# Performance work log

Hardware: AMD Instinct MI355X
Metric: run time of the kernel (lower is better)

## Reference

```python
import jax, jax.numpy as jnp
import numpy as np

C = 256        # in_channels
HEADS = 8
HD = 64        # dim_heads
INNER = HEADS * HD   # 512
G = 32         # norm_groups
FF = 4 * INNER # 2048
EPS = 1e-5


def setup_inputs() -> dict:
    key = jax.random.key(0)
    ks = jax.random.split(key, 12)
    r = lambda k, shp: jax.random.normal(k, shp, jnp.float32) * 0.02
    return {
        "x": jax.random.normal(ks[0], (1, C, 16, 16, 16), jnp.float32),
        "gn_g": jnp.ones((C,), jnp.float32),
        "gn_b": jnp.zeros((C,), jnp.float32),
        "w_in": r(ks[1], (INNER, C)),   # Conv3d 1x1x1 as (out,in) matrix
        "b_in": jnp.zeros((INNER,), jnp.float32),
        "wq": r(ks[2], (INNER, INNER)),
        "wk": r(ks[3], (INNER, INNER)),
        "wv": r(ks[4], (INNER, INNER)),
        "ln1_g": jnp.ones((INNER,), jnp.float32),
        "ln1_b": jnp.zeros((INNER,), jnp.float32),
        "ff_w1": r(ks[5], (FF, INNER)),
        "ff_b1": jnp.zeros((FF,), jnp.float32),
        "ff_w2": r(ks[6], (INNER, FF)),
        "ff_b2": jnp.zeros((INNER,), jnp.float32),
        "ln2_g": jnp.ones((INNER,), jnp.float32),
        "ln2_b": jnp.zeros((INNER,), jnp.float32),
        "w_out": r(ks[7], (C, INNER)),  # Conv3d 1x1x1 back to C
        "b_out": jnp.zeros((C,), jnp.float32),
    }


def _group_norm(x, g, b):
    # x: (B,C,D,H,W), G groups, normalize over (C//G, D, H, W)
    B, Cc, D, H, W = x.shape
    xr = x.reshape(B, G, Cc // G, D, H, W)
    mu = jnp.mean(xr, axis=(2, 3, 4, 5), keepdims=True)
    var = jnp.var(xr, axis=(2, 3, 4, 5), keepdims=True)
    xr = (xr - mu) * jax.lax.rsqrt(var + EPS)
    xn = xr.reshape(B, Cc, D, H, W)
    return xn * g[None, :, None, None, None] + b[None, :, None, None, None]


def _layer_norm(x, g, b):
    mu = jnp.mean(x, axis=-1, keepdims=True)
    var = jnp.var(x, axis=-1, keepdims=True)
    return (x - mu) * jax.lax.rsqrt(var + EPS) * g + b


def reference(x, gn_g, gn_b, w_in, b_in, wq, wk, wv, ln1_g, ln1_b,
              ff_w1, ff_b1, ff_w2, ff_b2, ln2_g, ln2_b, w_out, b_out):
    B, Cc, D, H, W = x.shape
    x_in = x
    # GroupNorm + proj_in (1x1x1 conv == channel matmul)
    h = _group_norm(x, gn_g, gn_b)
    t = jnp.einsum('bcdhw,oc->bodhw', h, w_in) + b_in[None, :, None, None, None]
    N = D * H * W
    t = t.reshape(B, INNER, N).transpose(0, 2, 1)  # (B, N, INNER)

    # self-attention (manual einsum softmax einsum)
    q = (t @ wq.T).reshape(B, N, HEADS, HD)
    k = (t @ wk.T).reshape(B, N, HEADS, HD)
    v = (t @ wv.T).reshape(B, N, HEADS, HD)
    scale = HD ** (-0.5)
    scores = jnp.einsum('bihd,bjhd->bhij', q, k) * scale  # (B,H,N,N)
    attn = jax.nn.softmax(scores, axis=-1)
    o = jnp.einsum('bhij,bjhd->bihd', attn, v).reshape(B, N, INNER)
    # out_proj is Identity (q_dim == inner_dim), dropout=0
    t = _layer_norm(o + t, ln1_g, ln1_b)

    # FeedForward: Linear -> GELU (erf) -> Linear
    ff = jax.nn.gelu(t @ ff_w1.T + ff_b1, approximate=False) @ ff_w2.T + ff_b2
    t = _layer_norm(ff + t, ln2_g, ln2_b)

    # proj_out + residual
    y = t.transpose(0, 2, 1).reshape(B, INNER, D, H, W)
    out = jnp.einsum('bidhw,oi->bodhw', y, w_out) + b_out[None, :, None, None, None]
    return out + x_in
```

## Files before the change

kernel.cpp:

```cpp
#include <hip/hip_runtime.h>
#include <hip/hip_bf16.h>

typedef unsigned short u16;
typedef __attribute__((ext_vector_type(8))) short short8;
typedef __attribute__((ext_vector_type(4))) float floatx4;

#define LOG2E 1.44269504088896f
#define CEXP (0.125f * LOG2E)

static __device__ __forceinline__ u16 f2b(float f) {
  union { float f; unsigned u; } v; v.f = f;
  unsigned r = v.u + 0x7fffu + ((v.u >> 16) & 1u);
  return (u16)(r >> 16);
}
static __device__ __forceinline__ float b2f(u16 b) {
  union { float f; unsigned u; } v; v.u = ((unsigned)b) << 16;
  return v.f;
}
static __device__ __forceinline__ void async16(const u16* g, u16* l) {
  __builtin_amdgcn_global_load_lds(
      (const __attribute__((address_space(1))) unsigned int*)g,
      (__attribute__((address_space(3))) unsigned int*)l, 16, 0, 0);
}
static __device__ __forceinline__ float fexp2(float x) {
  return __builtin_amdgcn_exp2f(x);
}

__global__ __launch_bounds__(256) void f2b_all(
    const float* __restrict__ s0, const float* __restrict__ s1, const float* __restrict__ s2,
    const float* __restrict__ s3, const float* __restrict__ s4, const float* __restrict__ s5,
    const float* __restrict__ s6, const float* __restrict__ x,
    u16* __restrict__ d_win, u16* __restrict__ d_qkv, u16* __restrict__ d_f1,
    u16* __restrict__ d_f2, u16* __restrict__ d_wout, float2* __restrict__ cstats) {
  if (blockIdx.x >= 12288) {
    int c = blockIdx.x - 12288;
    const float4* p4 = (const float4*)(x + (size_t)c * 4096);
    float s = 0.f, ss = 0.f;
#pragma unroll
    for (int j = 0; j < 4; j++) {
      float4 v = p4[j * 256 + threadIdx.x];
      s += v.x + v.y + v.z + v.w;
      ss += v.x * v.x + v.y * v.y + v.z * v.z + v.w * v.w;
    }
    for (int m = 1; m < 64; m <<= 1) { s += __shfl_xor(s, m); ss += __shfl_xor(ss, m); }
    __shared__ float sb[8];
    int w = threadIdx.x >> 6;
    if ((threadIdx.x & 63) == 0) { sb[w * 2] = s; sb[w * 2 + 1] = ss; }
    __syncthreads();
    if (threadIdx.x == 0)
      cstats[c] = float2{sb[0] + sb[2] + sb[4] + sb[6], sb[1] + sb[3] + sb[5] + sb[7]};
    return;
  }
  int i = blockIdx.x * 256 + threadIdx.x;
  if (i < 131072) { d_win[i] = f2b(s0[i]); return; }
  i -= 131072;
  if (i < 262144) { d_qkv[i] = f2b(s1[i]); return; }
  i -= 262144;
  if (i < 262144) { d_qkv[262144 + i] = f2b(s2[i]); return; }
  i -= 262144;
  if (i < 262144) { d_qkv[524288 + i] = f2b(s3[i]); return; }
  i -= 262144;
  if (i < 1048576) { d_f1[i] = f2b(s4[i]); return; }
  i -= 1048576;
  if (i < 1048576) { d_f2[i] = f2b(s5[i]); return; }
  i -= 1048576;
  d_wout[i] = f2b(s6[i]);
}

__global__ __launch_bounds__(256) void gn_apply(const float* __restrict__ x, const float2* __restrict__ cstats,
                                                const float* __restrict__ gg, const float* __restrict__ gb,
                                                u16* __restrict__ hn) {
  __shared__ float tile[256 * 17];
  __shared__ float gmu[32], grs[32];
  int t = threadIdx.x;
  if (t < 32) {
    float s = 0.f, ss = 0.f;
#pragma unroll
    for (int j = 0; j < 8; j++) { float2 p = cstats[t * 8 + j]; s += p.x; ss += p.y; }
    float mu = s / 32768.f;
    gmu[t] = mu;
    grs[t] = rsqrtf(ss / 32768.f - mu * mu + 1e-5f);
  }
  __syncthreads();
  int n0 = blockIdx.x * 16;
#pragma unroll
  for (int j = 0; j < 4; j++) {
    int c = j * 64 + (t >> 2);
    int nl = (t & 3) * 4;
    float4 v = *(const float4*)&x[(size_t)c * 4096 + n0 + nl];
    float ga = gg[c] * grs[c >> 3];
    float bb = gb[c] - gmu[c >> 3] * ga;
    tile[c * 17 + nl + 0] = v.x * ga + bb;
    tile[c * 17 + nl + 1] = v.y * ga + bb;
    tile[c * 17 + nl + 2] = v.z * ga + bb;
    tile[c * 17 + nl + 3] = v.w * ga + bb;
  }
  __syncthreads();
#pragma unroll
  for (int j = 0; j < 16; j++)
    hn[(size_t)(n0 + j) * 256 + t] = f2b(tile[t * 17 + j]);
}

#define FLAG_BIAS 1
#define FLAG_GELU 2
#define FLAG_C16 8
#define FLAG_FINAL 32
#define FLAG_CZ 64

__global__ __launch_bounds__(256) void gemm_bt(
    const u16* __restrict__ A, const u16* __restrict__ B, const float* __restrict__ bias,
    float* __restrict__ C32, u16* __restrict__ C16, const float* __restrict__ resid,
    int M, int N, int K, int flags) {
  __shared__ u16 As[128 * 64];
  __shared__ u16 Bs[64 * 64];
  const int t = threadIdx.x;
  const int lane = t & 63;
  const int w = t >> 6;
  const int ln = lane & 15;
  const int quad = lane >> 4;
  const int m0 = blockIdx.x * 128;
  const int n0 = blockIdx.y * 64;
  const int wm = (w >> 1) * 64;
  const int wn = (w & 1) * 32;

  floatx4 acc[4][2];
#pragma unroll
  for (int i = 0; i < 4; i++)
#pragma unroll
    for (int j = 0; j < 2; j++) acc[i][j] = floatx4{0.f, 0.f, 0.f, 0.f};

  for (int k0 = 0; k0 < K; k0 += 64) {
    __syncthreads();
#pragma unroll
    for (int i = 0; i < 4; ++i) {
      int s = i * 256 + t;
      int row = s >> 3;
      int kb = (s & 7) ^ (row & 7);
      async16(A + (size_t)(m0 + row) * K + k0 + kb * 8, &As[(i * 256 + (t & ~63)) * 8]);
    }
#pragma unroll
    for (int i = 0; i < 2; ++i) {
      int s = i * 256 + t;
      int row = s >> 3;
      int kb = (s & 7) ^ (row & 7);
      async16(B + (size_t)(n0 + row) * K + k0 + kb * 8, &Bs[(i * 256 + (t & ~63)) * 8]);
    }
    __syncthreads();
#pragma unroll
    for (int ksi = 0; ksi < 2; ksi++) {
      short8 af[4], bfr[2];
      int kb = ksi * 4 + quad;
#pragma unroll
      for (int i = 0; i < 4; i++) {
        int m = wm + i * 16 + ln;
        af[i] = *(const short8*)&As[(m * 8 + (kb ^ (m & 7))) * 8];
      }
#pragma unroll
      for (int j = 0; j < 2; j++) {
        int n = wn + j * 16 + ln;
        bfr[j] = *(const short8*)&Bs[(n * 8 + (kb ^ (n & 7))) * 8];
      }
#pragma unroll
      for (int i = 0; i < 4; i++)
#pragma unroll
        for (int j = 0; j < 2; j++)
          acc[i][j] = __builtin_amdgcn_mfma_f32_16x16x32_bf16(af[i], bfr[j], acc[i][j], 0, 0, 0);
    }
  }

#pragma unroll
  for (int i = 0; i < 4; i++) {
#pragma unroll
    for (int j = 0; j < 2; j++) {
      int n = n0 + wn + j * 16 + ln;
      float bv = (flags & FLAG_BIAS) ? bias[n] : 0.f;
#pragma unroll
      for (int r = 0; r < 4; r++) {
        int m = m0 + wm + i * 16 + quad * 4 + r;
        float v = acc[i][j][r] + bv;
        if (flags & FLAG_C16) C16[(size_t)m * N + n] = f2b(v);
        if (flags & FLAG_FINAL)
          C32[(size_t)m * N + n] = v + bias[m] + resid[(size_t)m * N + n];
      }
    }
  }
}

__global__ __launch_bounds__(256) void gemm_big(
    const u16* __restrict__ A, const u16* __restrict__ B, const float* __restrict__ bias,
    u16* __restrict__ C16, int M, int N, int K, int flags) {
  __shared__ u16 As[128 * 64];
  __shared__ u16 Bs[128 * 64];
  const int t = threadIdx.x;
  const int lane = t & 63;
  const int w = t >> 6;
  const int ln = lane & 15;
  const int quad = lane >> 4;
  const int m0 = blockIdx.x * 128;
  const int n0 = blockIdx.y * 128;
  const int wm = (w >> 1) * 64;
  const int wn = (w & 1) * 64;
  const int kper = K / gridDim.z;
  const int kbeg = blockIdx.z * kper;

  floatx4 acc[4][4];
#pragma unroll
  for (int i = 0; i < 4; i++)
#pragma unroll
    for (int j = 0; j < 4; j++) acc[i][j] = floatx4{0.f, 0.f, 0.f, 0.f};

  for (int k0 = kbeg; k0 < kbeg + kper; k0 += 64) {
    __syncthreads();
#pragma unroll
    for (int i = 0; i < 4; ++i) {
      int s = i * 256 + t;
      int row = s >> 3;
      int kb = (s & 7) ^ (row & 7);
      async16(A + (size_t)(m0 + row) * K + k0 + kb * 8, &As[(i * 256 + (t & ~63)) * 8]);
      async16(B + (size_t)(n0 + row) * K + k0 + kb * 8, &Bs[(i * 256 + (t & ~63)) * 8]);
    }
    __syncthreads();
#pragma unroll
    for (int ksi = 0; ksi < 2; ksi++) {
      short8 af[4], bfr[4];
      int kb = ksi * 4 + quad;
#pragma unroll
      for (int i = 0; i < 4; i++) {
        int m = wm + i * 16 + ln;
        af[i] = *(const short8*)&As[(m * 8 + (kb ^ (m & 7))) * 8];
        int n = wn + i * 16 + ln;
        bfr[i] = *(const short8*)&Bs[(n * 8 + (kb ^ (n & 7))) * 8];
      }
#pragma unroll
      for (int i = 0; i < 4; i++)
#pragma unroll
        for (int j = 0; j < 4; j++)
          acc[i][j] = __builtin_amdgcn_mfma_f32_16x16x32_bf16(af[i], bfr[j], acc[i][j], 0, 0, 0);
    }
  }

  u16* Cdst = (flags & FLAG_CZ) ? C16 + (size_t)blockIdx.z * M * N : C16;
#pragma unroll
  for (int i = 0; i < 4; i++) {
#pragma unroll
    for (int j = 0; j < 4; j++) {
      int n = n0 + wn + j * 16 + ln;
      float bv = ((flags & FLAG_BIAS) && blockIdx.z == 0) ? bias[n] : 0.f;
#pragma unroll
      for (int r = 0; r < 4; r++) {
        int m = m0 + wm + i * 16 + quad * 4 + r;
        float v = acc[i][j][r] + bv;
        if (flags & FLAG_GELU) v = 0.5f * v * (1.f + erff(v * 0.70710678118f));
        Cdst[(size_t)m * N + n] = f2b(v);
      }
    }
  }
}

__global__ __launch_bounds__(256) void gemm_qk(
    const u16* __restrict__ A, const u16* __restrict__ B,
    u16* __restrict__ Cq, u16* __restrict__ Ck, int M, int K) {
  __shared__ u16 As[64 * 64];
  __shared__ u16 Bs[128 * 64];
  const int t = threadIdx.x;
  const int lane = t & 63;
  const int w = t >> 6;
  const int ln = lane & 15;
  const int quad = lane >> 4;
  const int m0 = blockIdx.x * 64;
  const int n0 = blockIdx.y * 128;
  const int wm = (w >> 1) * 32;
  const int wn = (w & 1) * 64;

  floatx4 acc[2][4];
#pragma unroll
  for (int i = 0; i < 2; i++)
#pragma unroll
    for (int j = 0; j < 4; j++) acc[i][j] = floatx4{0.f, 0.f, 0.f, 0.f};

  for (int k0 = 0; k0 < K; k0 += 64) {
    __syncthreads();
#pragma unroll
    for (int i = 0; i < 2; ++i) {
      int s = i * 256 + t;
      int row = s >> 3;
      int kb = (s & 7) ^ (row & 7);
      async16(A + (size_t)(m0 + row) * K + k0 + kb * 8, &As[(i * 256 + (t & ~63)) * 8]);
    }
#pragma unroll
    for (int i = 0; i < 4; ++i) {
      int s = i * 256 + t;
      int row = s >> 3;
      int kb = (s & 7) ^ (row & 7);
      async16(B + (size_t)(n0 + row) * K + k0 + kb * 8, &Bs[(i * 256 + (t & ~63)) * 8]);
    }
    __syncthreads();
#pragma unroll
    for (int ksi = 0; ksi < 2; ksi++) {
      short8 af[2], bfr[4];
      int kb = ksi * 4 + quad;
#pragma unroll
      for (int i = 0; i < 2; i++) {
        int m = wm + i * 16 + ln;
        af[i] = *(const short8*)&As[(m * 8 + (kb ^ (m & 7))) * 8];
      }
#pragma unroll
      for (int j = 0; j < 4; j++) {
        int n = wn + j * 16 + ln;
        bfr[j] = *(const short8*)&Bs[(n * 8 + (kb ^ (n & 7))) * 8];
      }
#pragma unroll
      for (int i = 0; i < 2; i++)
#pragma unroll
        for (int j = 0; j < 4; j++)
          acc[i][j] = __builtin_amdgcn_mfma_f32_16x16x32_bf16(af[i], bfr[j], acc[i][j], 0, 0, 0);
    }
  }

#pragma unroll
  for (int i = 0; i < 2; i++) {
#pragma unroll
    for (int j = 0; j < 4; j++) {
      int n = n0 + wn + j * 16 + ln;
#pragma unroll
      for (int r = 0; r < 4; r++) {
        int m = m0 + wm + i * 16 + quad * 4 + r;
        float v = acc[i][j][r];
        if (n < 512) Cq[(size_t)m * 512 + n] = f2b(v * CEXP);
        else Ck[(size_t)m * 512 + (n - 512)] = f2b(v);
      }
    }
  }
}

__global__ __launch_bounds__(256, 4) void attn_kernel(
    const u16* __restrict__ Q, const u16* __restrict__ Km, const u16* __restrict__ VT,
    u16* __restrict__ Opart, float* __restrict__ ML, int Nseq, int kvLen) {
  __shared__ u16 Ks[64 * 64];
  __shared__ u16 Vs[64 * 64];
  __shared__ u16 Ps[4 * 32 * 64];
  const int t = threadIdx.x;
  const int lane = t & 63;
  const int w = t >> 6;
  const int ln = lane & 15;
  const int quad = lane >> 4;
  const int h = blockIdx.y;
  const int q0 = blockIdx.x * 128;
  const int split = blockIdx.z;
  const int kvbase = split * kvLen;
  u16* Opw = Opart + (size_t)split * Nseq * 512;
  u16* Pw = &Ps[w * 32 * 64];

  short8 qf[2][2];
#pragma unroll
  for (int qt = 0; qt < 2; qt++)
#pragma unroll
    for (int ksi = 0; ksi < 2; ksi++)
      qf[qt][ksi] = *(const short8*)&Q[(size_t)(q0 + w * 32 + qt * 16 + ln) * 512 + h * 64 + ksi * 32 + quad * 8];

  floatx4 accO[2][4];
#pragma unroll
  for (int qt = 0; qt < 2; qt++)
#pragma unroll
    for (int td = 0; td < 4; td++) accO[qt][td] = floatx4{0.f, 0.f, 0.f, 0.f};
  float lsum[2] = {0.f, 0.f};

  for (int kv = 0; kv < kvLen; kv += 64) {
    const int kv0 = kvbase + kv;
    __syncthreads();
#pragma unroll
    for (int i = 0; i < 2; ++i) {
      int s = i * 256 + t;
      int row = s >> 3;
      int kb = (s & 7) ^ (row & 7);
      async16(Km + (size_t)(kv0 + row) * 512 + h * 64 + kb * 8, &Ks[(i * 256 + (t & ~63)) * 8]);
      async16(VT + (size_t)(h * 64 + row) * Nseq + kv0 + kb * 8, &Vs[(i * 256 + (t & ~63)) * 8]);
    }
    __syncthreads();

    floatx4 accS[2][4];
#pragma unroll
    for (int qt = 0; qt < 2; qt++)
#pragma unroll
      for (int tj = 0; tj < 4; tj++) accS[qt][tj] = floatx4{0.f, 0.f, 0.f, 0.f};
#pragma unroll
    for (int ksi = 0; ksi < 2; ksi++) {
      int kb = ksi * 4 + quad;
      short8 kf[4];
#pragma unroll
      for (int tj = 0; tj < 4; tj++) {
        int key = tj * 16 + ln;
        kf[tj] = *(const short8*)&Ks[(key * 8 + (kb ^ (key & 7))) * 8];
      }
#pragma unroll
      for (int qt = 0; qt < 2; qt++)
#pragma unroll
        for (int tj = 0; tj < 4; tj++)
          accS[qt][tj] = __builtin_amdgcn_mfma_f32_16x16x32_bf16(kf[tj], qf[qt][ksi], accS[qt][tj], 0, 0, 0);
    }

#pragma unroll
    for (int qt = 0; qt < 2; qt++) {
      int q8 = (qt * 16 + ln) * 8;
#pragma unroll
      for (int tj = 0; tj < 4; tj++) {
        float p0 = fexp2(accS[qt][tj][0]);
        float p1 = fexp2(accS[qt][tj][1]);
        float p2 = fexp2(accS[qt][tj][2]);
        float p3 = fexp2(accS[qt][tj][3]);
        lsum[qt] += (p0 + p1) + (p2 + p3);
        __hip_bfloat162 a01 = __float22bfloat162_rn(float2{p0, p1});
        __hip_bfloat162 a23 = __float22bfloat162_rn(float2{p2, p3});
        uint2 pk;
        pk.x = *(unsigned*)&a01;
        pk.y = *(unsigned*)&a23;
        int kbx = tj * 2 + (quad >> 1);
        *(uint2*)&Pw[(q8 + (kbx ^ (ln & 7))) * 8 + (quad & 1) * 4] = pk;
      }
    }

#pragma unroll
    for (int ksi = 0; ksi < 2; ksi++) {
      int kb = ksi * 4 + quad;
      short8 pf[2];
#pragma unroll
      for (int qt = 0; qt < 2; qt++)
        pf[qt] = *(const short8*)&Pw[((qt * 16 + ln) * 8 + (kb ^ (ln & 7))) * 8];
#pragma unroll
      for (int td = 0; td < 4; td++) {
        int d = td * 16 + ln;
        short8 vf = *(const short8*)&Vs[(d * 8 + (kb ^ (d & 7))) * 8];
#pragma unroll
        for (int qt = 0; qt < 2; qt++)
          accO[qt][td] = __builtin_amdgcn_mfma_f32_16x16x32_bf16(vf, pf[qt], accO[qt][td], 0, 0, 0);
      }
    }
  }

#pragma unroll
  for (int qt = 0; qt < 2; qt++) {
    lsum[qt] += __shfl_xor(lsum[qt], 16);
    lsum[qt] += __shfl_xor(lsum[qt], 32);
  }
#pragma unroll
  for (int qt = 0; qt < 2; qt++) {
    int q = q0 + w * 32 + qt * 16 + ln;
#pragma unroll
    for (int td = 0; td < 4; td++) {
      __hip_bfloat162 p01 = __float22bfloat162_rn(float2{accO[qt][td][0], accO[qt][td][1]});
      __hip_bfloat162 p23 = __float22bfloat162_rn(float2{accO[qt][td][2], accO[qt][td][3]});
      uint2 pk;
      pk.x = *(unsigned*)&p01;
      pk.y = *(unsigned*)&p23;
      *(uint2*)&Opw[(size_t)q * 512 + h * 64 + td * 16 + quad * 4] = pk;
    }
    if (quad == 0)
      ML[((size_t)split * 8 + h) * Nseq + q] = lsum[qt];
  }
}

__global__ __launch_bounds__(256) void ln_attn(
    const u16* __restrict__ Opart, const float* __restrict__ ML,
    const u16* __restrict__ t16, const float* __restrict__ g, const float* __restrict__ be,
    u16* __restrict__ o16) {
  int row = blockIdx.x;
  int t = threadIdx.x;
  size_t base = (size_t)row * 512;
  int c0 = 2 * t;
  int h = c0 >> 6;
  float lt = 0.f;
#pragma unroll
  for (int s = 0; s < 4; s++) lt += ML[((size_t)s * 8 + h) * 4096 + row];
  float a0 = 0.f, a1 = 0.f;
#pragma unroll
  for (int s = 0; s < 4; s++) {
    unsigned oo = *(const unsigned*)&Opart[(size_t)s * 4096 * 512 + base + c0];
    a0 += b2f((u16)(oo & 0xffff));
    a1 += b2f((u16)(oo >> 16));
  }
  unsigned tt = *(const unsigned*)&t16[base + c0];
  float inv = 1.0f / lt;
  float v0 = a0 * inv + b2f((u16)(tt & 0xffff));
  float v1 = a1 * inv + b2f((u16)(tt >> 16));
  float s = v0 + v1, ss = v0 * v0 + v1 * v1;
  for (int m = 1; m < 64; m <<= 1) { s += __shfl_xor(s, m); ss += __shfl_xor(ss, m); }
  __shared__ float sb[8];
  int w = t >> 6;
  if ((t & 63) == 0) { sb[w * 2] = s; sb[w * 2 + 1] = ss; }
  __syncthreads();
  s = sb[0] + sb[2] + sb[4] + sb[6];
  ss = sb[1] + sb[3] + sb[5] + sb[7];
  float mu = s / 512.f;
  float var = ss / 512.f - mu * mu;
  float rs = rsqrtf(var + 1e-5f);
  float2 gv = *(const float2*)&g[c0];
  float2 bv = *(const float2*)&be[c0];
  u16 r0 = f2b((v0 - mu) * rs * gv.x + bv.x);
  u16 r1 = f2b((v1 - mu) * rs * gv.y + bv.y);
  *(unsigned*)&o16[base + c0] = ((unsigned)r1 << 16) | r0;
}

__global__ __launch_bounds__(256) void ln_ff(
    const u16* __restrict__ zp, const u16* __restrict__ u,
    const float* __restrict__ g, const float* __restrict__ be, u16* __restrict__ o16) {
  int row = blockIdx.x;
  int t = threadIdx.x;
  size_t base = (size_t)row * 512;
  int c0 = 2 * t;
  unsigned uu = *(const unsigned*)&u[base + c0];
  float v0 = b2f((u16)(uu & 0xffff));
  float v1 = b2f((u16)(uu >> 16));
#pragma unroll
  for (int z = 0; z < 4; z++) {
    unsigned zz = *(const unsigned*)&zp[(size_t)z * 4096 * 512 + base + c0];
    v0 += b2f((u16)(zz & 0xffff));
    v1 += b2f((u16)(zz >> 16));
  }
  float s = v0 + v1, ss = v0 * v0 + v1 * v1;
  for (int m = 1; m < 64; m <<= 1) { s += __shfl_xor(s, m); ss += __shfl_xor(ss, m); }
  __shared__ float sb[8];
  int w = t >> 6;
  if ((t & 63) == 0) { sb[w * 2] = s; sb[w * 2 + 1] = ss; }
  __syncthreads();
  s = sb[0] + sb[2] + sb[4] + sb[6];
  ss = sb[1] + sb[3] + sb[5] + sb[7];
  float mu = s / 512.f;
  float var = ss / 512.f - mu * mu;
  float rs = rsqrtf(var + 1e-5f);
  float2 gv = *(const float2*)&g[c0];
  float2 bv = *(const float2*)&be[c0];
  u16 r0 = f2b((v0 - mu) * rs * gv.x + bv.x);
  u16 r1 = f2b((v1 - mu) * rs * gv.y + bv.y);
  *(unsigned*)&o16[base + c0] = ((unsigned)r1 << 16) | r0;
}

extern "C" void kernel_launch(void* const* d_in, const int* in_sizes, int n_in,
                              void* d_out, int out_size, void* d_ws, size_t ws_size,
                              hipStream_t stream) {
  const float* x = (const float*)d_in[0];
  const float* gn_g = (const float*)d_in[1];
  const float* gn_b = (const float*)d_in[2];
  const float* w_in = (const float*)d_in[3];
  const float* b_in = (const float*)d_in[4];
  const float* wq = (const float*)d_in[5];
  const float* wk = (const float*)d_in[6];
  const float* wv = (const float*)d_in[7];
  const float* ln1_g = (const float*)d_in[8];
  const float* ln1_b = (const float*)d_in[9];
  const float* ff_w1 = (const float*)d_in[10];
  const float* ff_b1 = (const float*)d_in[11];
  const float* ff_w2 = (const float*)d_in[12];
  const float* ff_b2 = (const float*)d_in[13];
  const float* ln2_g = (const float*)d_in[14];
  const float* ln2_b = (const float*)d_in[15];
  const float* w_out = (const float*)d_in[16];
  const float* b_out = (const float*)d_in[17];
  float* out = (float*)d_out;
  char* ws = (char*)d_ws;

  u16* w_in16 = (u16*)(ws + 0);
  u16* wqkv16 = (u16*)(ws + 262144);
  u16* fw116 = (u16*)(ws + 1835008);
  u16* fw216 = (u16*)(ws + 3932160);
  u16* wout16 = (u16*)(ws + 6029312);
  u16* u16b = (u16*)(ws + 6291456);
  u16* zp = (u16*)(ws + 10485760);
  u16* t16 = (u16*)(ws + 14680064);
  u16* qb = (u16*)(ws + 18874368);
  u16* kb = (u16*)(ws + 23068672);
  u16* vt = (u16*)(ws + 27262976);
  u16* zb = (u16*)(ws + 27262976);
  u16* opart = (u16*)(ws + 31457280);
  u16* g16 = (u16*)(ws + 31457280);
  float* ml = (float*)(ws + 48234496);
  u16* hn = (u16*)(ws + 49283072);
  float2* cstats = (float2*)(ws + 51380224);

  f2b_all<<<12544, 256, 0, stream>>>(w_in, wq, wk, wv, ff_w1, ff_w2, w_out, x,
                                     w_in16, wqkv16, fw116, fw216, wout16, cstats);
  gn_apply<<<256, 256, 0, stream>>>(x, cstats, gn_g, gn_b, hn);

  gemm_bt<<<dim3(32, 8), 256, 0, stream>>>(hn, w_in16, b_in, nullptr, t16, nullptr,
                                           4096, 512, 256, FLAG_BIAS | FLAG_C16);
  gemm_qk<<<dim3(64, 8), 256, 0, stream>>>(t16, wqkv16, qb, kb, 4096, 512);
  gemm_bt<<<dim3(4, 64), 256, 0, stream>>>(wqkv16 + 2 * 512 * 512, t16, nullptr, nullptr, vt, nullptr,
                                           512, 4096, 512, FLAG_C16);
  attn_kernel<<<dim3(32, 8, 4), 256, 0, stream>>>(qb, kb, vt, opart, ml, 4096, 1024);
  ln_attn<<<4096, 256, 0, stream>>>(opart, ml, t16, ln1_g, ln1_b, u16b);
  gemm_big<<<dim3(32, 16), 256, 0, stream>>>(u16b, fw116, ff_b1, g16,
                                             4096, 2048, 512, FLAG_BIAS | FLAG_GELU | FLAG_C16);
  gemm_big<<<dim3(32, 4, 4), 256, 0, stream>>>(g16, fw216, ff_b2, zp,
                                               4096, 512, 2048, FLAG_BIAS | FLAG_CZ);
  ln_ff<<<4096, 256, 0, stream>>>(zp, u16b, ln2_g, ln2_b, zb);
  gemm_bt<<<dim3(2, 64), 256, 0, stream>>>(wout16, zb, b_out, out, nullptr, x,
                                           256, 4096, 512, FLAG_FINAL);
}
```

Baseline: 245.2 us.

## Merge QK and V-transpose GEMMs into one launch; enlarge attention query tile

Fuses the Q/K projection GEMM and the transposed V projection GEMM into a single kernel launch with 768 blocks, where each block picks its operands from its block index. This removes one launch and lets the two GEMMs share the GPU. The attention kernel now handles 256 queries per block (64 per wave) instead of 128, so each K/V tile loaded into LDS is reused across twice as many queries. In exchange the kernel uses more registers and LDS (launch_bounds min-occupancy dropped) and launches half as many blocks (512), which may lower occupancy.

```diff
diff --git a/kernel.cpp b/kernel.cpp
--- a/kernel.cpp
+++ b/kernel.cpp
@@ -257,9 +257,9 @@
   }
 }
 
-__global__ __launch_bounds__(256) void gemm_qk(
-    const u16* __restrict__ A, const u16* __restrict__ B,
-    u16* __restrict__ Cq, u16* __restrict__ Ck, int M, int K) {
+__global__ __launch_bounds__(256) void gemm_qkvt(
+    const u16* __restrict__ T, const u16* __restrict__ Wqkv,
+    u16* __restrict__ Cq, u16* __restrict__ Ck, u16* __restrict__ CvT) {
   __shared__ u16 As[64 * 64];
   __shared__ u16 Bs[128 * 64];
   const int t = threadIdx.x;
@@ -267,8 +267,23 @@
   const int w = t >> 6;
   const int ln = lane & 15;
   const int quad = lane >> 4;
-  const int m0 = blockIdx.x * 64;
-  const int n0 = blockIdx.y * 128;
+  const int bx = blockIdx.x;
+  const bool isv = bx >= 512;
+  const u16* A;
+  const u16* B;
+  int m0, n0;
+  if (!isv) {
+    m0 = (bx >> 3) * 64;
+    n0 = (bx & 7) * 128;
+    A = T;
+    B = Wqkv;
+  } else {
+    int b2 = bx - 512;
+    m0 = (b2 >> 5) * 64;
+    n0 = (b2 & 31) * 128;
+    A = Wqkv + 2 * 512 * 512;
+    B = T;
+  }
   const int wm = (w >> 1) * 32;
   const int wn = (w & 1) * 64;
 
@@ -278,21 +293,21 @@
 #pragma unroll
     for (int j = 0; j < 4; j++) acc[i][j] = floatx4{0.f, 0.f, 0.f, 0.f};
 
-  for (int k0 = 0; k0 < K; k0 += 64) {
+  for (int k0 = 0; k0 < 512; k0 += 64) {
     __syncthreads();
 #pragma unroll
     for (int i = 0; i < 2; ++i) {
       int s = i * 256 + t;
       int row = s >> 3;
       int kb = (s & 7) ^ (row & 7);
-      async16(A + (size_t)(m0 + row) * K + k0 + kb * 8, &As[(i * 256 + (t & ~63)) * 8]);
+      async16(A + (size_t)(m0 + row) * 512 + k0 + kb * 8, &As[(i * 256 + (t & ~63)) * 8]);
     }
 #pragma unroll
     for (int i = 0; i < 4; ++i) {
       int s = i * 256 + t;
       int row = s >> 3;
       int kb = (s & 7) ^ (row & 7);
-      async16(B + (size_t)(n0 + row) * K + k0 + kb * 8, &Bs[(i * 256 + (t & ~63)) * 8]);
+      async16(B + (size_t)(n0 + row) * 512 + k0 + kb * 8, &Bs[(i * 256 + (t & ~63)) * 8]);
     }
     __syncthreads();
 #pragma unroll
@@ -326,44 +341,45 @@
       for (int r = 0; r < 4; r++) {
         int m = m0 + wm + i * 16 + quad * 4 + r;
         float v = acc[i][j][r];
-        if (n < 512) Cq[(size_t)m * 512 + n] = f2b(v * CEXP);
+        if (isv) CvT[(size_t)m * 4096 + n] = f2b(v);
+        else if (n < 512) Cq[(size_t)m * 512 + n] = f2b(v * CEXP);
         else Ck[(size_t)m * 512 + (n - 512)] = f2b(v);
       }
     }
   }
 }
 
-__global__ __launch_bounds__(256, 4) void attn_kernel(
+__global__ __launch_bounds__(256) void attn_kernel(
     const u16* __restrict__ Q, const u16* __restrict__ Km, const u16* __restrict__ VT,
     u16* __restrict__ Opart, float* __restrict__ ML, int Nseq, int kvLen) {
   __shared__ u16 Ks[64 * 64];
   __shared__ u16 Vs[64 * 64];
-  __shared__ u16 Ps[4 * 32 * 64];
+  __shared__ u16 Ps[4 * 64 * 64];
   const int t = threadIdx.x;
   const int lane = t & 63;
   const int w = t >> 6;
   const int ln = lane & 15;
   const int quad = lane >> 4;
   const int h = blockIdx.y;
-  const int q0 = blockIdx.x * 128;
+  const int q0 = blockIdx.x * 256;
   const int split = blockIdx.z;
   const int kvbase = split * kvLen;
   u16* Opw = Opart + (size_t)split * Nseq * 512;
-  u16* Pw = &Ps[w * 32 * 64];
-
-  short8 qf[2][2];
-#pragma unroll
-  for (int qt = 0; qt < 2; qt++)
+  u16* Pw = &Ps[w * 64 * 64];
+
+  short8 qf[4][2];
+#pragma unroll
+  for (int qt = 0; qt < 4; qt++)
 #pragma unroll
     for (int ksi = 0; ksi < 2; ksi++)
-      qf[qt][ksi] = *(const short8*)&Q[(size_t)(q0 + w * 32 + qt * 16 + ln) * 512 + h * 64 + ksi * 32 + quad * 8];
-
-  floatx4 accO[2][4];
-#pragma unroll
-  for (int qt = 0; qt < 2; qt++)
+      qf[qt][ksi] = *(const short8*)&Q[(size_t)(q0 + w * 64 + qt * 16 + ln) * 512 + h * 64 + ksi * 32 + quad * 8];
+
+  floatx4 accO[4][4];
+#pragma unroll
+  for (int qt = 0; qt < 4; qt++)
 #pragma unroll
     for (int td = 0; td < 4; td++) accO[qt][td] = floatx4{0.f, 0.f, 0.f, 0.f};
-  float lsum[2] = {0.f, 0.f};
+  float lsum[4] = {0.f, 0.f, 0.f, 0.f};
 
   for (int kv = 0; kv < kvLen; kv += 64) {
     const int kv0 = kvbase + kv;
@@ -378,36 +394,34 @@
     }
     __syncthreads();
 
-    floatx4 accS[2][4];
-#pragma unroll
-    for (int qt = 0; qt < 2; qt++)
-#pragma unroll
-      for (int tj = 0; tj < 4; tj++) accS[qt][tj] = floatx4{0.f, 0.f, 0.f, 0.f};
+    short8 kf[2][4];
 #pragma unroll
     for (int ksi = 0; ksi < 2; ksi++) {
       int kb = ksi * 4 + quad;
-      short8 kf[4];
 #pragma unroll
       for (int tj = 0; tj < 4; tj++) {
         int key = tj * 16 + ln;
-        kf[tj] = *(const short8*)&Ks[(key * 8 + (kb ^ (key & 7))) * 8];
-      }
-#pragma unroll
-      for (int qt = 0; qt < 2; qt++)
+        kf[ksi][tj] = *(const short8*)&Ks[(key * 8 + (kb ^ (key & 7))) * 8];
+      }
+    }
+
+#pragma unroll
+    for (int qt = 0; qt < 4; qt++) {
+      floatx4 accS[4];
+#pragma unroll
+      for (int tj = 0; tj < 4; tj++) accS[tj] = floatx4{0.f, 0.f, 0.f, 0.f};
+#pragma unroll
+      for (int ksi = 0; ksi < 2; ksi++)
 #pragma unroll
         for (int tj = 0; tj < 4; tj++)
-          accS[qt][tj] = __builtin_amdgcn_mfma_f32_16x16x32_bf16(kf[tj], qf[qt][ksi], accS[qt][tj], 0, 0, 0);
-    }
-
-#pragma unroll
-    for (int qt = 0; qt < 2; qt++) {
+          accS[tj] = __builtin_amdgcn_mfma_f32_16x16x32_bf16(kf[ksi][tj], qf[qt][ksi], accS[tj], 0, 0, 0);
       int q8 = (qt * 16 + ln) * 8;
 #pragma unroll
       for (int tj = 0; tj < 4; tj++) {
-        float p0 = fexp2(accS[qt][tj][0]);
-        float p1 = fexp2(accS[qt][tj][1]);
-        float p2 = fexp2(accS[qt][tj][2]);
-        float p3 = fexp2(accS[qt][tj][3]);
+        float p0 = fexp2(accS[tj][0]);
+        float p1 = fexp2(accS[tj][1]);
+        float p2 = fexp2(accS[tj][2]);
+        float p3 = fexp2(accS[tj][3]);
         lsum[qt] += (p0 + p1) + (p2 + p3);
         __hip_bfloat162 a01 = __float22bfloat162_rn(float2{p0, p1});
         __hip_bfloat162 a23 = __float22bfloat162_rn(float2{p2, p3});
@@ -422,29 +436,29 @@
 #pragma unroll
     for (int ksi = 0; ksi < 2; ksi++) {
       int kb = ksi * 4 + quad;
-      short8 pf[2];
-#pragma unroll
-      for (int qt = 0; qt < 2; qt++)
+      short8 pf[4];
+#pragma unroll
+      for (int qt = 0; qt < 4; qt++)
         pf[qt] = *(const short8*)&Pw[((qt * 16 + ln) * 8 + (kb ^ (ln & 7))) * 8];
 #pragma unroll
       for (int td = 0; td < 4; td++) {
         int d = td * 16 + ln;
         short8 vf = *(const short8*)&Vs[(d * 8 + (kb ^ (d & 7))) * 8];
 #pragma unroll
-        for (int qt = 0; qt < 2; qt++)
+        for (int qt = 0; qt < 4; qt++)
           accO[qt][td] = __builtin_amdgcn_mfma_f32_16x16x32_bf16(vf, pf[qt], accO[qt][td], 0, 0, 0);
       }
     }
   }
 
 #pragma unroll
-  for (int qt = 0; qt < 2; qt++) {
+  for (int qt = 0; qt < 4; qt++) {
     lsum[qt] += __shfl_xor(lsum[qt], 16);
     lsum[qt] += __shfl_xor(lsum[qt], 32);
   }
 #pragma unroll
-  for (int qt = 0; qt < 2; qt++) {
-    int q = q0 + w * 32 + qt * 16 + ln;
+  for (int qt = 0; qt < 4; qt++) {
+    int q = q0 + w * 64 + qt * 16 + ln;
 #pragma unroll
     for (int td = 0; td < 4; td++) {
       __hip_bfloat162 p01 = __float22bfloat162_rn(float2{accO[qt][td][0], accO[qt][td][1]});
@@ -582,10 +596,8 @@
 
   gemm_bt<<<dim3(32, 8), 256, 0, stream>>>(hn, w_in16, b_in, nullptr, t16, nullptr,
                                            4096, 512, 256, FLAG_BIAS | FLAG_C16);
-  gemm_qk<<<dim3(64, 8), 256, 0, stream>>>(t16, wqkv16, qb, kb, 4096, 512);
-  gemm_bt<<<dim3(4, 64), 256, 0, stream>>>(wqkv16 + 2 * 512 * 512, t16, nullptr, nullptr, vt, nullptr,
-                                           512, 4096, 512, FLAG_C16);
-  attn_kernel<<<dim3(32, 8, 4), 256, 0, stream>>>(qb, kb, vt, opart, ml, 4096, 1024);
+  gemm_qkvt<<<768, 256, 0, stream>>>(t16, wqkv16, qb, kb, vt);
+  attn_kernel<<<dim3(16, 8, 4), 256, 0, stream>>>(qb, kb, vt, opart, ml, 4096, 1024);
   ln_attn<<<4096, 256, 0, stream>>>(opart, ml, t16, ln1_g, ln1_b, u16b);
   gemm_big<<<dim3(32, 16), 256, 0, stream>>>(u16b, fw116, ff_b1, g16,
                                              4096, 2048, 512, FLAG_BIAS | FLAG_GELU | FLAG_C16);
```

Measured after the change: 257.0 us. 4.8% more time.

## Vectorize weight casts, merge QK and V^T GEMMs, add smaller-tile output GEMM

Applied to the files above, without the earlier changes.

The fp32-to-bf16 weight conversion now processes four elements per thread with float4 loads and ushort4 stores, cutting the block count by four. The separate Q/K projection GEMM and the V-transpose GEMM are merged into one launch of 768 blocks that picks operands by block index, removing one launch and letting both run concurrently. The final projection moves from a 128x64-tile GEMM with 128 blocks to a dedicated 64x64-tile kernel with 256 blocks to fill more compute units, at the cost of less data reuse per block.

```diff
diff --git a/kernel.cpp b/kernel.cpp
--- a/kernel.cpp
+++ b/kernel.cpp
@@ -32,8 +32,8 @@
     const float* __restrict__ s6, const float* __restrict__ x,
     u16* __restrict__ d_win, u16* __restrict__ d_qkv, u16* __restrict__ d_f1,
     u16* __restrict__ d_f2, u16* __restrict__ d_wout, float2* __restrict__ cstats) {
-  if (blockIdx.x >= 12288) {
-    int c = blockIdx.x - 12288;
+  if (blockIdx.x >= 3072) {
+    int c = blockIdx.x - 3072;
     const float4* p4 = (const float4*)(x + (size_t)c * 4096);
     float s = 0.f, ss = 0.f;
 #pragma unroll
@@ -52,19 +52,19 @@
     return;
   }
   int i = blockIdx.x * 256 + threadIdx.x;
-  if (i < 131072) { d_win[i] = f2b(s0[i]); return; }
-  i -= 131072;
-  if (i < 262144) { d_qkv[i] = f2b(s1[i]); return; }
-  i -= 262144;
-  if (i < 262144) { d_qkv[262144 + i] = f2b(s2[i]); return; }
-  i -= 262144;
-  if (i < 262144) { d_qkv[524288 + i] = f2b(s3[i]); return; }
-  i -= 262144;
-  if (i < 1048576) { d_f1[i] = f2b(s4[i]); return; }
-  i -= 1048576;
-  if (i < 1048576) { d_f2[i] = f2b(s5[i]); return; }
-  i -= 1048576;
-  d_wout[i] = f2b(s6[i]);
+  const float* src;
+  u16* dst;
+  if (i < 32768) { src = s0; dst = d_win; }
+  else if ((i -= 32768) < 65536) { src = s1; dst = d_qkv; }
+  else if ((i -= 65536) < 65536) { src = s2; dst = d_qkv + 262144; }
+  else if ((i -= 65536) < 65536) { src = s3; dst = d_qkv + 524288; }
+  else if ((i -= 65536) < 262144) { src = s4; dst = d_f1; }
+  else if ((i -= 262144) < 262144) { src = s5; dst = d_f2; }
+  else { i -= 262144; src = s6; dst = d_wout; }
+  float4 v = *(const float4*)&src[i * 4];
+  ushort4 o;
+  o.x = f2b(v.x); o.y = f2b(v.y); o.z = f2b(v.z); o.w = f2b(v.w);
+  *(ushort4*)&dst[i * 4] = o;
 }
 
 __global__ __launch_bounds__(256) void gn_apply(const float* __restrict__ x, const float2* __restrict__ cstats,
@@ -104,13 +104,11 @@
 #define FLAG_BIAS 1
 #define FLAG_GELU 2
 #define FLAG_C16 8
-#define FLAG_FINAL 32
 #define FLAG_CZ 64
 
 __global__ __launch_bounds__(256) void gemm_bt(
     const u16* __restrict__ A, const u16* __restrict__ B, const float* __restrict__ bias,
-    float* __restrict__ C32, u16* __restrict__ C16, const float* __restrict__ resid,
-    int M, int N, int K, int flags) {
+    u16* __restrict__ C16, int M, int N, int K, int flags) {
   __shared__ u16 As[128 * 64];
   __shared__ u16 Bs[64 * 64];
   const int t = threadIdx.x;
@@ -179,8 +177,77 @@
         int m = m0 + wm + i * 16 + quad * 4 + r;
         float v = acc[i][j][r] + bv;
         if (flags & FLAG_C16) C16[(size_t)m * N + n] = f2b(v);
-        if (flags & FLAG_FINAL)
-          C32[(size_t)m * N + n] = v + bias[m] + resid[(size_t)m * N + n];
+      }
+    }
+  }
+}
+
+__global__ __launch_bounds__(256) void gemm_out(
+    const u16* __restrict__ A, const u16* __restrict__ B, const float* __restrict__ brow,
+    const float* __restrict__ resid, float* __restrict__ C32, int N, int K) {
+  __shared__ u16 As[64 * 64];
+  __shared__ u16 Bs[64 * 64];
+  const int t = threadIdx.x;
+  const int lane = t & 63;
+  const int w = t >> 6;
+  const int ln = lane & 15;
+  const int quad = lane >> 4;
+  const int m0 = blockIdx.x * 64;
+  const int n0 = blockIdx.y * 64;
+  const int wm = (w >> 1) * 32;
+  const int wn = (w & 1) * 32;
+
+  floatx4 acc[2][2];
+#pragma unroll
+  for (int i = 0; i < 2; i++)
+#pragma unroll
+    for (int j = 0; j < 2; j++) acc[i][j] = floatx4{0.f, 0.f, 0.f, 0.f};
+
+  for (int k0 = 0; k0 < K; k0 += 64) {
+    __syncthreads();
+#pragma unroll
+    for (int i = 0; i < 2; ++i) {
+      int s = i * 256 + t;
+      int row = s >> 3;
+      int kb = (s & 7) ^ (row & 7);
+      async16(A + (size_t)(m0 + row) * K + k0 + kb * 8, &As[(i * 256 + (t & ~63)) * 8]);
+    }
+#pragma unroll
+    for (int i = 0; i < 2; ++i) {
+      int s = i * 256 + t;
+      int row = s >> 3;
+      int kb = (s & 7) ^ (row & 7);
+      async16(B + (size_t)(n0 + row) * K + k0 + kb * 8, &Bs[(i * 256 + (t & ~63)) * 8]);
+    }
+    __syncthreads();
+#pragma unroll
+    for (int ksi = 0; ksi < 2; ksi++) {
+      short8 af[2], bfr[2];
+      int kb = ksi * 4 + quad;
+#pragma unroll
+      for (int i = 0; i < 2; i++) {
+        int m = wm + i * 16 + ln;
+        af[i] = *(const short8*)&As[(m * 8 + (kb ^ (m & 7))) * 8];
+        int n = wn + i * 16 + ln;
+        bfr[i] = *(const short8*)&Bs[(n * 8 + (kb ^ (n & 7))) * 8];
+      }
+#pragma unroll
+      for (int i = 0; i < 2; i++)
+#pragma unroll
+        for (int j = 0; j < 2; j++)
+          acc[i][j] = __builtin_amdgcn_mfma_f32_16x16x32_bf16(af[i], bfr[j], acc[i][j], 0, 0, 0);
+    }
+  }
+
+#pragma unroll
+  for (int i = 0; i < 2; i++) {
+#pragma unroll
+    for (int j = 0; j < 2; j++) {
+      int n = n0 + wn + j * 16 + ln;
+#pragma unroll
+      for (int r = 0; r < 4; r++) {
+        int m = m0 + wm + i * 16 + quad * 4 + r;
+        C32[(size_t)m * N + n] = acc[i][j][r] + brow[m] + resid[(size_t)m * N + n];
       }
     }
   }
@@ -257,9 +324,9 @@
   }
 }
 
-__global__ __launch_bounds__(256) void gemm_qk(
-    const u16* __restrict__ A, const u16* __restrict__ B,
-    u16* __restrict__ Cq, u16* __restrict__ Ck, int M, int K) {
+__global__ __launch_bounds__(256) void gemm_qkvt(
+    const u16* __restrict__ T, const u16* __restrict__ Wqkv,
+    u16* __restrict__ Cq, u16* __restrict__ Ck, u16* __restrict__ CvT) {
   __shared__ u16 As[64 * 64];
   __shared__ u16 Bs[128 * 64];
   const int t = threadIdx.x;
@@ -267,8 +334,23 @@
   const int w = t >> 6;
   const int ln = lane & 15;
   const int quad = lane >> 4;
-  const int m0 = blockIdx.x * 64;
-  const int n0 = blockIdx.y * 128;
+  const int bx = blockIdx.x;
+  const bool isv = bx >= 512;
+  const u16* A;
+  const u16* B;
+  int m0, n0;
+  if (!isv) {
+    m0 = (bx >> 3) * 64;
+    n0 = (bx & 7) * 128;
+    A = T;
+    B = Wqkv;
+  } else {
+    int b2 = bx - 512;
+    m0 = (b2 >> 5) * 64;
+    n0 = (b2 & 31) * 128;
+    A = Wqkv + 2 * 512 * 512;
+    B = T;
+  }
   const int wm = (w >> 1) * 32;
   const int wn = (w & 1) * 64;
 
@@ -278,21 +360,21 @@
 #pragma unroll
     for (int j = 0; j < 4; j++) acc[i][j] = floatx4{0.f, 0.f, 0.f, 0.f};
 
-  for (int k0 = 0; k0 < K; k0 += 64) {
+  for (int k0 = 0; k0 < 512; k0 += 64) {
     __syncthreads();
 #pragma unroll
     for (int i = 0; i < 2; ++i) {
       int s = i * 256 + t;
       int row = s >> 3;
       int kb = (s & 7) ^ (row & 7);
-      async16(A + (size_t)(m0 + row) * K + k0 + kb * 8, &As[(i * 256 + (t & ~63)) * 8]);
+      async16(A + (size_t)(m0 + row) * 512 + k0 + kb * 8, &As[(i * 256 + (t & ~63)) * 8]);
     }
 #pragma unroll
     for (int i = 0; i < 4; ++i) {
       int s = i * 256 + t;
       int row = s >> 3;
       int kb = (s & 7) ^ (row & 7);
-      async16(B + (size_t)(n0 + row) * K + k0 + kb * 8, &Bs[(i * 256 + (t & ~63)) * 8]);
+      async16(B + (size_t)(n0 + row) * 512 + k0 + kb * 8, &Bs[(i * 256 + (t & ~63)) * 8]);
     }
     __syncthreads();
 #pragma unroll
@@ -326,7 +408,8 @@
       for (int r = 0; r < 4; r++) {
         int m = m0 + wm + i * 16 + quad * 4 + r;
         float v = acc[i][j][r];
-        if (n < 512) Cq[(size_t)m * 512 + n] = f2b(v * CEXP);
+        if (isv) CvT[(size_t)m * 4096 + n] = f2b(v);
+        else if (n < 512) Cq[(size_t)m * 512 + n] = f2b(v * CEXP);
         else Ck[(size_t)m * 512 + (n - 512)] = f2b(v);
       }
     }
@@ -576,15 +659,13 @@
   u16* hn = (u16*)(ws + 49283072);
   float2* cstats = (float2*)(ws + 51380224);
 
-  f2b_all<<<12544, 256, 0, stream>>>(w_in, wq, wk, wv, ff_w1, ff_w2, w_out, x,
-                                     w_in16, wqkv16, fw116, fw216, wout16, cstats);
+  f2b_all<<<3328, 256, 0, stream>>>(w_in, wq, wk, wv, ff_w1, ff_w2, w_out, x,
+                                    w_in16, wqkv16, fw116, fw216, wout16, cstats);
   gn_apply<<<256, 256, 0, stream>>>(x, cstats, gn_g, gn_b, hn);
 
-  gemm_bt<<<dim3(32, 8), 256, 0, stream>>>(hn, w_in16, b_in, nullptr, t16, nullptr,
+  gemm_bt<<<dim3(32, 8), 256, 0, stream>>>(hn, w_in16, b_in, t16,
                                            4096, 512, 256, FLAG_BIAS | FLAG_C16);
-  gemm_qk<<<dim3(64, 8), 256, 0, stream>>>(t16, wqkv16, qb, kb, 4096, 512);
-  gemm_bt<<<dim3(4, 64), 256, 0, stream>>>(wqkv16 + 2 * 512 * 512, t16, nullptr, nullptr, vt, nullptr,
-                                           512, 4096, 512, FLAG_C16);
+  gemm_qkvt<<<768, 256, 0, stream>>>(t16, wqkv16, qb, kb, vt);
   attn_kernel<<<dim3(32, 8, 4), 256, 0, stream>>>(qb, kb, vt, opart, ml, 4096, 1024);
   ln_attn<<<4096, 256, 0, stream>>>(opart, ml, t16, ln1_g, ln1_b, u16b);
   gemm_big<<<dim3(32, 16), 256, 0, stream>>>(u16b, fw116, ff_b1, g16,
@@ -592,6 +673,5 @@
   gemm_big<<<dim3(32, 4, 4), 256, 0, stream>>>(g16, fw216, ff_b2, zp,
                                                4096, 512, 2048, FLAG_BIAS | FLAG_CZ);
   ln_ff<<<4096, 256, 0, stream>>>(zp, u16b, ln2_g, ln2_b, zb);
-  gemm_bt<<<dim3(2, 64), 256, 0, stream>>>(wout16, zb, b_out, out, nullptr, x,
-                                           256, 4096, 512, FLAG_FINAL);
-}
+  gemm_out<<<dim3(4, 64), 256, 0, stream>>>(wout16, zb, b_out, x, out, 4096, 512);
+}
```

Measured after the change: 224.9 us. 1.09x faster.
